# Performance work log

Hardware: AMD Instinct MI355X
Metric: run time of the kernel (lower is better)

The kernel has to match this reference:

```python
import jax, jax.numpy as jnp
import numpy as np

H = 16       # query heads
KV = 4       # key/value heads
HD = 256     # head dim
ROPE_THETA = 10000.0
EPS = 1e-6


def _rms_norm(x, w):
    # Gemma RMSNorm over last dim: x / rms * (1 + w), computed in fp32
    xf = x.astype(jnp.float32)
    var = jnp.mean(xf * xf, axis=-1, keepdims=True)
    out = xf * jax.lax.rsqrt(var + EPS) * (1.0 + w.astype(jnp.float32))
    return out.astype(x.dtype)


def _rope_cos_sin(position_ids):
    # cos/sin tables of shape [S, HD]
    inv_freq = 1.0 / (ROPE_THETA ** (jnp.arange(0, HD, 2, dtype=jnp.float32) / HD))
    ang = position_ids.astype(jnp.float32)[:, None] * inv_freq[None, :]  # [S, HD/2]
    emb = jnp.concatenate([ang, ang], axis=-1)                           # [S, HD]
    return jnp.cos(emb), jnp.sin(emb)


def _rotate_half(x):
    x1, x2 = jnp.split(x, 2, axis=-1)
    return jnp.concatenate([-x2, x1], axis=-1)


def _apply_rope(x, cos, sin):
    # x: [B, h, S, HD]; cos/sin: [S, HD] -> broadcast over batch and heads
    c = cos[None, None, :, :]
    s = sin[None, None, :, :]
    return (x * c + _rotate_half(x) * s).astype(x.dtype)


def setup_inputs() -> dict:
    key = jax.random.key(0)
    ks = jax.random.split(key, 8)
    B, S, D = 2, 2048, 2048
    inp = {
        "hidden_states": jax.random.normal(ks[0], (B, S, D), jnp.float32),
        "Wq": jax.random.normal(ks[1], (D, H * HD), jnp.float32) * 0.02,
        "Wk": jax.random.normal(ks[2], (D, KV * HD), jnp.float32) * 0.02,
        "Wv": jax.random.normal(ks[3], (D, KV * HD), jnp.float32) * 0.02,
        "Wo": jax.random.normal(ks[4], (H * HD, D), jnp.float32) * 0.02,
        "q_norm_w": jnp.zeros((HD,), jnp.float32),
        "k_norm_w": jnp.zeros((HD,), jnp.float32),
        "position_ids": jnp.arange(S, dtype=jnp.int32),
    }
    return inp


def reference(hidden_states, Wq, Wk, Wv, Wo, q_norm_w, k_norm_w, position_ids):
    B, S, D = hidden_states.shape
    scale = HD ** -0.5

    # projections -> [B, h, S, HD]
    q = jnp.einsum("bsd,de->bse", hidden_states, Wq).reshape(B, S, H, HD).transpose(0, 2, 1, 3)
    k = jnp.einsum("bsd,de->bse", hidden_states, Wk).reshape(B, S, KV, HD).transpose(0, 2, 1, 3)
    v = jnp.einsum("bsd,de->bse", hidden_states, Wv).reshape(B, S, KV, HD).transpose(0, 2, 1, 3)

    # Gemma per-head RMSNorm on q/k
    q = _rms_norm(q, q_norm_w)
    k = _rms_norm(k, k_norm_w)

    # RoPE
    cos, sin = _rope_cos_sin(position_ids)
    q = _apply_rope(q, cos, sin)
    k = _apply_rope(k, cos, sin)

    # GQA: repeat kv heads to match query heads
    rep = H // KV
    k = jnp.repeat(k, rep, axis=1)  # [B, H, S, HD]
    v = jnp.repeat(v, rep, axis=1)

    # SDPA with causal mask, softmax in fp32
    scores = jnp.einsum("bhqd,bhkd->bhqk", q, k) * scale
    causal = jnp.tril(jnp.ones((S, S), dtype=bool))
    scores = jnp.where(causal[None, None, :, :], scores, jnp.finfo(jnp.float32).min)
    probs = jax.nn.softmax(scores.astype(jnp.float32), axis=-1).astype(q.dtype)
    attn = jnp.einsum("bhqk,bhkd->bhqd", probs, v)  # [B, H, S, HD]

    attn = attn.transpose(0, 2, 1, 3).reshape(B, S, H * HD)
    return jnp.einsum("bse,ed->bsd", attn, Wo)
```

## Files before the change

kernel.cpp:

```cpp
#include <hip/hip_runtime.h>

typedef unsigned short ushort_t;
typedef __bf16 bf16_t;
typedef bf16_t bf16x8 __attribute__((ext_vector_type(8)));
typedef float floatx4 __attribute__((ext_vector_type(4)));
typedef ushort_t ushort4v __attribute__((ext_vector_type(4)));
typedef ushort_t ushort8v __attribute__((ext_vector_type(8)));

static constexpr int B = 2, S = 2048, D = 2048;
static constexpr int H = 16, KVH = 4, HD = 256;

#define DEVFN static __device__ __forceinline__

DEVFN ushort_t f2b(float f) {
  union { float f; unsigned u; } x; x.f = f;
  unsigned r = x.u + 0x7fffu + ((x.u >> 16) & 1u);
  return (ushort_t)(r >> 16);
}
DEVFN float b2f(ushort_t h) {
  union { unsigned u; float f; } x; x.u = ((unsigned)h) << 16;
  return x.f;
}
DEVFN void gll16(const void* g, void* l) {
  __builtin_amdgcn_global_load_lds(
      (const __attribute__((address_space(1))) void*)g,
      (__attribute__((address_space(3))) void*)l, 16, 0, 0);
}

DEVFN void bar() {
  asm volatile("" ::: "memory");
  __builtin_amdgcn_s_barrier();
  asm volatile("" ::: "memory");
}
template <int N>
DEVFN void waitvm() { asm volatile("s_waitcnt vmcnt(%0)" ::"n"(N) : "memory"); }

DEVFN ushort4v norm_rope_row(ushort4v raw, const float* __restrict__ w,
                             const float* __restrict__ tab, int s, float scale, int lane) {
  float v[4];
  float ss = 0.f;
#pragma unroll
  for (int i = 0; i < 4; i++) { v[i] = b2f(raw[i]); ss += v[i] * v[i]; }
#pragma unroll
  for (int m = 1; m < 64; m <<= 1) ss += __shfl_xor(ss, m, 64);
  const float inv = rsqrtf(ss * (1.0f / HD) + 1e-6f);
  float4 wv = *(const float4*)(w + lane * 4);
  float y[4];
  y[0] = v[0] * inv * (1.0f + wv.x);
  y[1] = v[1] * inv * (1.0f + wv.y);
  y[2] = v[2] * inv * (1.0f + wv.z);
  y[3] = v[3] * inv * (1.0f + wv.w);
  float py[4];
#pragma unroll
  for (int i = 0; i < 4; i++) py[i] = __shfl_xor(y[i], 32, 64);
  const bool lo = (lane < 32);
  ushort4v ov;
#pragma unroll
  for (int i = 0; i < 4; i++) {
    int dd = (lane * 4 + i) & 127;
    float2 cs = *(const float2*)(tab + ((size_t)s * 128 + dd) * 2);
    float rot = lo ? -py[i] : py[i];
    ov[i] = f2b((y[i] * cs.x + rot * cs.y) * scale);
  }
  return ov;
}

__global__ void k_cvt_bf16(const float* __restrict__ in, ushort_t* __restrict__ out, int n) {
  int i = (blockIdx.x * 256 + threadIdx.x) * 4;
  if (i >= n) return;
  float4 v = *(const float4*)(in + i);
  ushort4v o;
  o[0] = f2b(v.x); o[1] = f2b(v.y); o[2] = f2b(v.z); o[3] = f2b(v.w);
  *(ushort4v*)(out + i) = o;
}

__global__ void k_transpose_cvt(const float* __restrict__ in, ushort_t* __restrict__ out,
                                int R, int C) {
  __shared__ float tile[64][65];
  const int cb = blockIdx.x * 64, rb = blockIdx.y * 64;
  const int t = threadIdx.x;
  const int l16 = t & 15, g16 = t >> 4;
#pragma unroll
  for (int p = 0; p < 4; p++) {
    const int r = p * 16 + g16;
    float4 v = *(const float4*)(in + (size_t)(rb + r) * C + cb + l16 * 4);
    tile[r][l16 * 4 + 0] = v.x;
    tile[r][l16 * 4 + 1] = v.y;
    tile[r][l16 * 4 + 2] = v.z;
    tile[r][l16 * 4 + 3] = v.w;
  }
  __syncthreads();
#pragma unroll
  for (int p = 0; p < 4; p++) {
    const int c = p * 16 + g16;
    ushort4v o4;
#pragma unroll
    for (int i = 0; i < 4; i++) o4[i] = f2b(tile[l16 * 4 + i][c]);
    *(ushort4v*)(out + (size_t)(cb + c) * R + rb + l16 * 4) = o4;
  }
}

__global__ void k_rope_table(const int* __restrict__ pos_ids, float* __restrict__ tab) {
  int idx = blockIdx.x * 256 + threadIdx.x;
  int s = idx >> 7, dd = idx & 127;
  float ang = (float)pos_ids[s] * exp2f((float)dd * (-13.287712379549449f / 128.0f));
  tab[idx * 2] = cosf(ang);
  tab[idx * 2 + 1] = sinf(ang);
}

DEVFN void stage_tile(const ushort_t* __restrict__ A, const ushort_t* __restrict__ Bt,
                      ushort_t* smb, size_t arow0, size_t brow0, int K, int kt) {
  const int t = threadIdx.x;
  const int rq = t >> 2;
  const int cq = (t & 3) * 8;
#pragma unroll
  for (int i = 0; i < 2; i++) {
    const int cs = cq ^ ((rq & 8) << 1);
    gll16(A + (arow0 + rq) * (size_t)K + kt + i * 32 + cs, smb + i * 4096 + t * 8);
  }
#pragma unroll
  for (int i = 0; i < 4; i++) {
    const int row = ((i & 1) << 7) | rq;
    const int cs = cq ^ ((row & 8) << 1);
    gll16(Bt + (brow0 + row) * (size_t)K + kt + (i >> 1) * 32 + cs,
          smb + 8192 + i * 4096 + t * 8);
  }
}

DEVFN bf16x8 ldsA(const ushort_t* buf, int row, int ks, int lq) {
  const int c = (lq * 8) ^ ((row & 8) << 1);
  return *(const bf16x8*)(buf + ks * 4096 + row * 32 + c);
}
DEVFN bf16x8 ldsB(const ushort_t* buf, int row, int ks, int lq) {
  const int c = (lq * 8) ^ ((row & 8) << 1);
  return *(const bf16x8*)(buf + 8192 + ks * 8192 + row * 32 + c);
}

template <int MODE>
__global__ __launch_bounds__(512, 2)
void k_gemm256(const ushort_t* __restrict__ A, const ushort_t* __restrict__ Bt,
               void* __restrict__ C0, void* __restrict__ C1, void* __restrict__ C2,
               int N, int K) {
  __shared__ ushort_t sm[49152];
  const int tid = threadIdx.x;
  const int lane = tid & 63, wave = tid >> 6;
  const int lr = lane & 15, lq = lane >> 4;
  const int wm = wave >> 2, wn = wave & 3;
  const size_t m0 = (size_t)blockIdx.x * 128;
  const size_t n0 = (size_t)blockIdx.y * 256;

  floatx4 acc[4][4];
#pragma unroll
  for (int i = 0; i < 4; i++)
#pragma unroll
    for (int j = 0; j < 4; j++) acc[i][j] = {0.f, 0.f, 0.f, 0.f};

  const int NT = K >> 6;
  stage_tile(A, Bt, sm, m0, n0, K, 0);
  stage_tile(A, Bt, sm + 24576, m0, n0, K, 64);

  for (int t = 0; t < NT; ++t) {
    ushort_t* bA = sm + (t & 1) * 24576;
    if (t < NT - 1) waitvm<6>(); else waitvm<0>();
    bar();

    bf16x8 a[2][4], bfr[2][4];
#pragma unroll
    for (int ks = 0; ks < 2; ks++) {
#pragma unroll
      for (int m = 0; m < 4; m++) a[ks][m] = ldsA(bA, wm * 64 + m * 16 + lr, ks, lq);
#pragma unroll
      for (int n = 0; n < 4; n++) bfr[ks][n] = ldsB(bA, wn * 64 + n * 16 + lr, ks, lq);
    }
    __builtin_amdgcn_s_setprio(1);
#pragma unroll
    for (int m = 0; m < 4; m++)
#pragma unroll
      for (int n = 0; n < 4; n++)
        acc[m][n] = __builtin_amdgcn_mfma_f32_16x16x32_bf16(a[0][m], bfr[0][n], acc[m][n], 0, 0, 0);
    __builtin_amdgcn_s_setprio(0);
    asm volatile("s_waitcnt lgkmcnt(0)" ::: "memory");
    __builtin_amdgcn_sched_barrier(0);
    bar();
    if (t + 2 < NT) stage_tile(A, Bt, bA, m0, n0, K, (t + 2) * 64);
    __builtin_amdgcn_sched_barrier(0);
    __builtin_amdgcn_s_setprio(1);
#pragma unroll
    for (int m = 0; m < 4; m++)
#pragma unroll
      for (int n = 0; n < 4; n++)
        acc[m][n] = __builtin_amdgcn_mfma_f32_16x16x32_bf16(a[1][m], bfr[1][n], acc[m][n], 0, 0, 0);
    __builtin_amdgcn_s_setprio(0);
  }

  const int colb = (int)n0;
#pragma unroll
  for (int mg = 0; mg < 4; mg++)
#pragma unroll
    for (int ng = 0; ng < 4; ng++) {
      const size_t row0 = m0 + wm * 64 + mg * 16 + lq * 4;
      const int col = colb + wn * 64 + ng * 16 + lr;
      if (MODE == 1) {
#pragma unroll
        for (int r = 0; r < 4; r++)
          ((float*)C0)[(row0 + r) * N + col] = acc[mg][ng][r];
      } else {
        if (colb < 4096) {
#pragma unroll
          for (int r = 0; r < 4; r++)
            ((ushort_t*)C0)[(row0 + r) * 4096 + col] = f2b(acc[mg][ng][r]);
        } else if (colb < 5120) {
#pragma unroll
          for (int r = 0; r < 4; r++)
            ((ushort_t*)C1)[(row0 + r) * 1024 + (col - 4096)] = f2b(acc[mg][ng][r]);
        } else {
          const int ch = col - 5120;
          const int kvh = ch >> 8, chh = ch & 255, f = chh >> 4, lrv = chh & 15;
          const size_t bb = row0 >> 11;
          const int s0 = (int)(row0 & 2047);
          const int tile = s0 >> 6, kh = (s0 >> 5) & 1, lqv = (s0 >> 3) & 3, j0 = s0 & 7;
          ushort4v pk;
#pragma unroll
          for (int r = 0; r < 4; r++) pk[r] = f2b(acc[mg][ng][r]);
          *(ushort4v*)&((ushort_t*)C2)[((bb * KVH + kvh) * (S / 64) + tile) * 16384 +
                                       (size_t)(f * 2 + kh) * 512 +
                                       (size_t)(lqv * 16 + lrv) * 8 + j0] = pk;
        }
      }
    }
}

__global__ void k_norm_rope_k(const ushort_t* __restrict__ Kb, ushort_t* __restrict__ Kf,
                              const float* __restrict__ w, const float* __restrict__ tab) {
  __shared__ ushort_t t[64 * 264];
  const int lane = threadIdx.x & 63, wave = threadIdx.x >> 6;
  const int tile = blockIdx.x, kvh = blockIdx.y, b = blockIdx.z;
#pragma unroll
  for (int rr = 0; rr < 16; rr++) {
    const int row = wave * 16 + rr;
    const int s = tile * 64 + row;
    const ushort_t* p = Kb + ((size_t)(b * S + s) * KVH + kvh) * HD + lane * 4;
    ushort4v raw = *(const ushort4v*)p;
    *(ushort4v*)&t[row * 264 + lane * 4] = norm_rope_row(raw, w, tab, s, 1.0f, lane);
  }
  __syncthreads();
  ushort_t* dst = Kf + ((size_t)(b * KVH + kvh) * (S / 64) + tile) * 16384;
  const int lr = lane & 15, lq = lane >> 4;
#pragma unroll
  for (int q = 0; q < 8; q++) {
    const int c = wave * 8 + q;
    const int nt = c >> 3, ks = c & 7;
    ushort8v v = *(const ushort8v*)&t[(nt * 16 + lr) * 264 + ks * 32 + lq * 8];
    *(ushort8v*)&dst[(size_t)c * 512 + lane * 8] = v;
  }
}

__global__ __launch_bounds__(256, 2)
void k_attn(const ushort_t* __restrict__ Q, const ushort_t* __restrict__ Kf,
            const ushort_t* __restrict__ Vf, ushort_t* __restrict__ O,
            const float* __restrict__ qw, const float* __restrict__ tab) {
  __shared__ ushort_t Ks[32 * 512];
  __shared__ ushort_t Vs[32 * 512];
  __shared__ ushort_t Ps[4][16 * 72];
  const int lane = threadIdx.x & 63, wave = threadIdx.x >> 6;
  const int lr = lane & 15, lq = lane >> 4;
  const int lin = blockIdx.x;
  const int g = lin & 7, j = lin >> 3;
  const int b = g >> 2, kvh = g & 3;
  const int h = kvh * 4 + (j >> 4);
  const int xq = j & 15;
  const size_t kvb = (size_t)(b * KVH + kvh) * (S / 64);

#pragma unroll 1
  for (int half = 0; half < 2; half++) {
    const int qt = half ? xq : (S / 64 - 1 - xq);
    const int q0 = qt * 64 + wave * 16;
    const int sq = q0 + lr;

    bf16x8 qf[8];
    {
      const ushort_t* qp = Q + ((size_t)(b * S + sq) * H + h) * HD + lq * 8;
      ushort8v qr[8];
#pragma unroll
      for (int ks = 0; ks < 8; ks++) qr[ks] = *(const ushort8v*)(qp + ks * 32);
      float ss = 0.f;
#pragma unroll
      for (int ks = 0; ks < 8; ks++)
#pragma unroll
        for (int jj = 0; jj < 8; jj++) { float v = b2f(qr[ks][jj]); ss += v * v; }
      ss += __shfl_xor(ss, 16, 64);
      ss += __shfl_xor(ss, 32, 64);
      const float inv = rsqrtf(ss * (1.0f / HD) + 1e-6f);
      const float sc = 0.0625f * 1.4426950408889634f;
#pragma unroll
      for (int c = 0; c < 4; c++) {
        const int d0 = c * 32 + lq * 8;
        float wl[8], wh[8];
        {
          float4 a0 = *(const float4*)(qw + d0);
          float4 a1 = *(const float4*)(qw + d0 + 4);
          float4 a2 = *(const float4*)(qw + d0 + 128);
          float4 a3 = *(const float4*)(qw + d0 + 132);
          wl[0]=a0.x; wl[1]=a0.y; wl[2]=a0.z; wl[3]=a0.w;
          wl[4]=a1.x; wl[5]=a1.y; wl[6]=a1.z; wl[7]=a1.w;
          wh[0]=a2.x; wh[1]=a2.y; wh[2]=a2.z; wh[3]=a2.w;
          wh[4]=a3.x; wh[5]=a3.y; wh[6]=a3.z; wh[7]=a3.w;
        }
        const float* tp = tab + ((size_t)sq * 128 + d0) * 2;
        ushort8v olo, ohi;
#pragma unroll
        for (int jj = 0; jj < 8; jj++) {
          float ylo = b2f(qr[c][jj]) * inv * (1.0f + wl[jj]);
          float yhi = b2f(qr[c + 4][jj]) * inv * (1.0f + wh[jj]);
          float2 cs = *(const float2*)(tp + jj * 2);
          olo[jj] = f2b((ylo * cs.x - yhi * cs.y) * sc);
          ohi[jj] = f2b((yhi * cs.x + ylo * cs.y) * sc);
        }
        qf[c] = *reinterpret_cast<bf16x8*>(&olo);
        qf[c + 4] = *reinterpret_cast<bf16x8*>(&ohi);
      }
    }

    floatx4 o[16];
#pragma unroll
    for (int f = 0; f < 16; f++) o[f] = {0.f, 0.f, 0.f, 0.f};
    float m_i[4] = {-1e30f, -1e30f, -1e30f, -1e30f};
    float l_i[4] = {0.f, 0.f, 0.f, 0.f};

    const int ntiles = qt + 1;
    for (int kt = 0; kt < ntiles; kt++) {
      const int kbase = kt * 64;
      __syncthreads();
      const ushort_t* tb = Kf + (kvb + kt) * 16384;
      const ushort_t* vb = Vf + (kvb + kt) * 16384;
#pragma unroll
      for (int i = 0; i < 16; i++) {
        const int c = wave * 16 + i;
        if (c < 32) gll16(tb + (size_t)c * 512 + lane * 8, &Ks[c * 512 + lane * 8]);
        else        gll16(vb + (size_t)(c - 32) * 512 + lane * 8, &Vs[(c - 32) * 512 + lane * 8]);
      }
      __syncthreads();

      const int ntmax = min(4, ((q0 + 15 - kbase) >> 4) + 1);
      floatx4 sacc[4];
#pragma unroll
      for (int nt = 0; nt < 4; nt++) {
        if (nt < ntmax) {
          sacc[nt] = {0.f, 0.f, 0.f, 0.f};
#pragma unroll
          for (int ks = 0; ks < 8; ks++) {
            bf16x8 kf = *(const bf16x8*)&Ks[(nt * 8 + ks) * 512 + lane * 8];
            sacc[nt] = __builtin_amdgcn_mfma_f32_16x16x32_bf16(qf[ks], kf, sacc[nt], 0, 0, 0);
          }
        } else {
          sacc[nt] = {-1e30f, -1e30f, -1e30f, -1e30f};
        }
      }
      if (kbase + 63 > q0) {
#pragma unroll
        for (int nt = 0; nt < 4; nt++)
          if (nt < ntmax)
#pragma unroll
            for (int r = 0; r < 4; r++)
              if (kbase + nt * 16 + lr > q0 + lq * 4 + r) sacc[nt][r] = -1e30f;
      }
      float mt[4], alpha[4], rs[4];
#pragma unroll
      for (int r = 0; r < 4; r++)
        mt[r] = fmaxf(fmaxf(sacc[0][r], sacc[1][r]), fmaxf(sacc[2][r], sacc[3][r]));
#pragma unroll
      for (int m = 1; m < 16; m <<= 1)
#pragma unroll
        for (int r = 0; r < 4; r++) mt[r] = fmaxf(mt[r], __shfl_xor(mt[r], m, 64));
#pragma unroll
      for (int r = 0; r < 4; r++) {
        float mn = fmaxf(m_i[r], mt[r]);
        alpha[r] = exp2f(m_i[r] - mn);
        m_i[r] = mn;
      }
#pragma unroll
      for (int nt = 0; nt < 4; nt++)
#pragma unroll
        for (int r = 0; r < 4; r++) sacc[nt][r] = exp2f(sacc[nt][r] - m_i[r]);
#pragma unroll
      for (int r = 0; r < 4; r++)
        rs[r] = (sacc[0][r] + sacc[1][r]) + (sacc[2][r] + sacc[3][r]);
#pragma unroll
      for (int m = 1; m < 16; m <<= 1)
#pragma unroll
        for (int r = 0; r < 4; r++) rs[r] += __shfl_xor(rs[r], m, 64);
#pragma unroll
      for (int r = 0; r < 4; r++) l_i[r] = l_i[r] * alpha[r] + rs[r];
      if (__any((alpha[0] < 1.f) | (alpha[1] < 1.f) | (alpha[2] < 1.f) | (alpha[3] < 1.f))) {
#pragma unroll
        for (int f = 0; f < 16; f++) {
          o[f][0] *= alpha[0]; o[f][1] *= alpha[1];
          o[f][2] *= alpha[2]; o[f][3] *= alpha[3];
        }
      }
      ushort_t* psw = Ps[wave];
#pragma unroll
      for (int nt = 0; nt < 4; nt++)
#pragma unroll
        for (int r = 0; r < 4; r++)
          psw[(lq * 4 + r) * 72 + nt * 16 + lr] = f2b(sacc[nt][r]);
      bf16x8 pf0 = *(const bf16x8*)&psw[lr * 72 + lq * 8];
      bf16x8 pf1 = *(const bf16x8*)&psw[lr * 72 + 32 + lq * 8];
#pragma unroll
      for (int f = 0; f < 16; f++) {
        bf16x8 vf0 = *(const bf16x8*)&Vs[(f * 2 + 0) * 512 + lane * 8];
        o[f] = __builtin_amdgcn_mfma_f32_16x16x32_bf16(pf0, vf0, o[f], 0, 0, 0);
        bf16x8 vf1 = *(const bf16x8*)&Vs[(f * 2 + 1) * 512 + lane * 8];
        o[f] = __builtin_amdgcn_mfma_f32_16x16x32_bf16(pf1, vf1, o[f], 0, 0, 0);
      }
    }
    float invl[4];
#pragma unroll
    for (int r = 0; r < 4; r++) invl[r] = 1.0f / l_i[r];
#pragma unroll
    for (int f = 0; f < 16; f++)
#pragma unroll
      for (int r = 0; r < 4; r++)
        O[((size_t)(b * S + q0 + lq * 4 + r) * H + h) * HD + f * 16 + lr] =
            f2b(o[f][r] * invl[r]);
  }
}

extern "C" void kernel_launch(void* const* d_in, const int* in_sizes, int n_in,
                              void* d_out, int out_size, void* d_ws, size_t ws_size,
                              hipStream_t stream) {
  const float* hs = (const float*)d_in[0];
  const float* Wq = (const float*)d_in[1];
  const float* Wk = (const float*)d_in[2];
  const float* Wv = (const float*)d_in[3];
  const float* Wo = (const float*)d_in[4];
  const float* qw = (const float*)d_in[5];
  const float* kw = (const float*)d_in[6];
  const int* pos = (const int*)d_in[7];
  float* out = (float*)d_out;

  char* ws = (char*)d_ws;
  size_t off = 0;
  auto alloc = [&](size_t bytes) {
    void* p = ws + off;
    off += (bytes + 255) & ~(size_t)255;
    return p;
  };
  ushort_t* Xb   = (ushort_t*)alloc((size_t)B * S * D * 2);
  ushort_t* Wqt  = (ushort_t*)alloc((size_t)(H * HD) * D * 2);
  ushort_t* Wkvt = (ushort_t*)alloc((size_t)(2 * KVH * HD) * D * 2);
  ushort_t* Wot  = (ushort_t*)alloc((size_t)D * (H * HD) * 2);
  ushort_t* Qb   = (ushort_t*)alloc((size_t)B * S * H * HD * 2);
  ushort_t* Kf   = (ushort_t*)alloc((size_t)B * S * KVH * HD * 2);
  ushort_t* Vf   = (ushort_t*)alloc((size_t)B * S * KVH * HD * 2);
  ushort_t* Ab   = (ushort_t*)alloc((size_t)B * S * H * HD * 2);
  float*    tab  = (float*)alloc((size_t)S * 128 * 2 * sizeof(float));
  ushort_t* Kb = Ab;

  k_cvt_bf16<<<(B * S * D / 4 + 255) / 256, 256, 0, stream>>>(hs, Xb, B * S * D);
  k_transpose_cvt<<<dim3((H * HD) / 64, D / 64), 256, 0, stream>>>(Wq, Wqt, D, H * HD);
  k_transpose_cvt<<<dim3((KVH * HD) / 64, D / 64), 256, 0, stream>>>(Wk, Wkvt, D, KVH * HD);
  k_transpose_cvt<<<dim3((KVH * HD) / 64, D / 64), 256, 0, stream>>>(
      Wv, Wkvt + (size_t)(KVH * HD) * D, D, KVH * HD);
  k_transpose_cvt<<<dim3(D / 64, (H * HD) / 64), 256, 0, stream>>>(Wo, Wot, H * HD, D);
  k_rope_table<<<S * 128 / 256, 256, 0, stream>>>(pos, tab);

  k_gemm256<0><<<dim3((B * S) / 128, 6144 / 256), 512, 0, stream>>>(
      Xb, Wqt, Qb, Kb, Vf, 6144, D);

  k_norm_rope_k<<<dim3(S / 64, KVH, B), 256, 0, stream>>>(Kb, Kf, kw, tab);

  k_attn<<<512, 256, 0, stream>>>(Qb, Kf, Vf, Ab, qw, tab);

  k_gemm256<1><<<dim3((B * S) / 128, D / 256), 512, 0, stream>>>(
      Ab, Wot, out, nullptr, nullptr, D, H * HD);
}
```

Before: 505.1 us.

## Process two 16-row query fragments per wave to reuse each K/V tile

The attention kernel now gives each block a 128-row query tile, with each wave holding two 16-row Q fragments. Every K/V tile staged in LDS therefore feeds twice as many MFMAs, which halves K/V global-to-LDS traffic and barrier rounds per query row. The old loop that paired a long and a short causal tile inside one block is gone; each block now handles one tile chosen from a mirrored index. The cost is doubled accumulator and Q-fragment registers, which risks spills or lower occupancy, and less even per-block work under the causal mask.

```diff
diff --git a/kernel.cpp b/kernel.cpp
--- a/kernel.cpp
+++ b/kernel.cpp
@@ -265,164 +265,196 @@
   const int lane = threadIdx.x & 63, wave = threadIdx.x >> 6;
   const int lr = lane & 15, lq = lane >> 4;
   const int lin = blockIdx.x;
-  const int g = lin & 7, j = lin >> 3;
+  const int half_sel = lin >> 8;
+  const int r9 = lin & 255;
+  const int g = r9 & 7;
   const int b = g >> 2, kvh = g & 3;
-  const int h = kvh * 4 + (j >> 4);
-  const int xq = j & 15;
+  const int j = r9 >> 3;
+  const int h = kvh * 4 + (j >> 3);
+  const int p = j & 7;
+  const int qt = half_sel ? p : (15 - p);
   const size_t kvb = (size_t)(b * KVH + kvh) * (S / 64);
 
-#pragma unroll 1
-  for (int half = 0; half < 2; half++) {
-    const int qt = half ? xq : (S / 64 - 1 - xq);
-    const int q0 = qt * 64 + wave * 16;
-    const int sq = q0 + lr;
-
-    bf16x8 qf[8];
-    {
-      const ushort_t* qp = Q + ((size_t)(b * S + sq) * H + h) * HD + lq * 8;
-      ushort8v qr[8];
-#pragma unroll
-      for (int ks = 0; ks < 8; ks++) qr[ks] = *(const ushort8v*)(qp + ks * 32);
-      float ss = 0.f;
-#pragma unroll
-      for (int ks = 0; ks < 8; ks++)
-#pragma unroll
-        for (int jj = 0; jj < 8; jj++) { float v = b2f(qr[ks][jj]); ss += v * v; }
-      ss += __shfl_xor(ss, 16, 64);
-      ss += __shfl_xor(ss, 32, 64);
-      const float inv = rsqrtf(ss * (1.0f / HD) + 1e-6f);
-      const float sc = 0.0625f * 1.4426950408889634f;
-#pragma unroll
-      for (int c = 0; c < 4; c++) {
-        const int d0 = c * 32 + lq * 8;
-        float wl[8], wh[8];
-        {
-          float4 a0 = *(const float4*)(qw + d0);
-          float4 a1 = *(const float4*)(qw + d0 + 4);
-          float4 a2 = *(const float4*)(qw + d0 + 128);
-          float4 a3 = *(const float4*)(qw + d0 + 132);
-          wl[0]=a0.x; wl[1]=a0.y; wl[2]=a0.z; wl[3]=a0.w;
-          wl[4]=a1.x; wl[5]=a1.y; wl[6]=a1.z; wl[7]=a1.w;
-          wh[0]=a2.x; wh[1]=a2.y; wh[2]=a2.z; wh[3]=a2.w;
-          wh[4]=a3.x; wh[5]=a3.y; wh[6]=a3.z; wh[7]=a3.w;
+  const int q0 = qt * 128 + wave * 32;
+  const int ntiles = 2 * qt + 2;
+
+  bf16x8 qf[2][8];
+#pragma unroll
+  for (int rf = 0; rf < 2; rf++) {
+    const int sq = q0 + rf * 16 + lr;
+    const ushort_t* qp = Q + ((size_t)(b * S + sq) * H + h) * HD + lq * 8;
+    ushort8v qr[8];
+#pragma unroll
+    for (int ks = 0; ks < 8; ks++) qr[ks] = *(const ushort8v*)(qp + ks * 32);
+    float ss = 0.f;
+#pragma unroll
+    for (int ks = 0; ks < 8; ks++)
+#pragma unroll
+      for (int jj = 0; jj < 8; jj++) { float v = b2f(qr[ks][jj]); ss += v * v; }
+    ss += __shfl_xor(ss, 16, 64);
+    ss += __shfl_xor(ss, 32, 64);
+    const float inv = rsqrtf(ss * (1.0f / HD) + 1e-6f);
+    const float sc = 0.0625f * 1.4426950408889634f;
+#pragma unroll
+    for (int c = 0; c < 4; c++) {
+      const int d0 = c * 32 + lq * 8;
+      float wl[8], wh[8];
+      {
+        float4 a0 = *(const float4*)(qw + d0);
+        float4 a1 = *(const float4*)(qw + d0 + 4);
+        float4 a2 = *(const float4*)(qw + d0 + 128);
+        float4 a3 = *(const float4*)(qw + d0 + 132);
+        wl[0]=a0.x; wl[1]=a0.y; wl[2]=a0.z; wl[3]=a0.w;
+        wl[4]=a1.x; wl[5]=a1.y; wl[6]=a1.z; wl[7]=a1.w;
+        wh[0]=a2.x; wh[1]=a2.y; wh[2]=a2.z; wh[3]=a2.w;
+        wh[4]=a3.x; wh[5]=a3.y; wh[6]=a3.z; wh[7]=a3.w;
+      }
+      const float* tp = tab + ((size_t)sq * 128 + d0) * 2;
+      ushort8v olo, ohi;
+#pragma unroll
+      for (int jj = 0; jj < 8; jj++) {
+        float ylo = b2f(qr[c][jj]) * inv * (1.0f + wl[jj]);
+        float yhi = b2f(qr[c + 4][jj]) * inv * (1.0f + wh[jj]);
+        float2 cs = *(const float2*)(tp + jj * 2);
+        olo[jj] = f2b((ylo * cs.x - yhi * cs.y) * sc);
+        ohi[jj] = f2b((yhi * cs.x + ylo * cs.y) * sc);
+      }
+      qf[rf][c] = *reinterpret_cast<bf16x8*>(&olo);
+      qf[rf][c + 4] = *reinterpret_cast<bf16x8*>(&ohi);
+    }
+  }
+
+  floatx4 o[2][16];
+#pragma unroll
+  for (int rf = 0; rf < 2; rf++)
+#pragma unroll
+    for (int f = 0; f < 16; f++) o[rf][f] = {0.f, 0.f, 0.f, 0.f};
+  float m_i[2][4], l_i[2][4];
+#pragma unroll
+  for (int rf = 0; rf < 2; rf++)
+#pragma unroll
+    for (int r = 0; r < 4; r++) { m_i[rf][r] = -1e30f; l_i[rf][r] = 0.f; }
+
+  for (int kt = 0; kt < ntiles; kt++) {
+    const int kbase = kt * 64;
+    __syncthreads();
+    const ushort_t* tb = Kf + (kvb + kt) * 16384;
+    const ushort_t* vb = Vf + (kvb + kt) * 16384;
+#pragma unroll
+    for (int i = 0; i < 16; i++) {
+      const int c = wave * 16 + i;
+      if (c < 32) gll16(tb + (size_t)c * 512 + lane * 8, &Ks[c * 512 + lane * 8]);
+      else        gll16(vb + (size_t)(c - 32) * 512 + lane * 8, &Vs[(c - 32) * 512 + lane * 8]);
+    }
+    __syncthreads();
+
+    const int ntmax0 = min(4, ((q0 + 15 - kbase) >> 4) + 1);
+    const int ntmax1 = min(4, ((q0 + 31 - kbase) >> 4) + 1);
+    if (ntmax1 > 0) {
+      floatx4 sacc[2][4];
+#pragma unroll
+      for (int nt = 0; nt < 4; nt++) {
+        const bool a0 = nt < ntmax0, a1 = nt < ntmax1;
+        sacc[0][nt] = a0 ? floatx4{0.f, 0.f, 0.f, 0.f}
+                         : floatx4{-1e30f, -1e30f, -1e30f, -1e30f};
+        sacc[1][nt] = a1 ? floatx4{0.f, 0.f, 0.f, 0.f}
+                         : floatx4{-1e30f, -1e30f, -1e30f, -1e30f};
+        if (a1) {
+#pragma unroll
+          for (int ks = 0; ks < 8; ks++) {
+            bf16x8 kf = *(const bf16x8*)&Ks[(nt * 8 + ks) * 512 + lane * 8];
+            if (a0)
+              sacc[0][nt] = __builtin_amdgcn_mfma_f32_16x16x32_bf16(qf[0][ks], kf, sacc[0][nt], 0, 0, 0);
+            sacc[1][nt] = __builtin_amdgcn_mfma_f32_16x16x32_bf16(qf[1][ks], kf, sacc[1][nt], 0, 0, 0);
+          }
         }
-        const float* tp = tab + ((size_t)sq * 128 + d0) * 2;
-        ushort8v olo, ohi;
-#pragma unroll
-        for (int jj = 0; jj < 8; jj++) {
-          float ylo = b2f(qr[c][jj]) * inv * (1.0f + wl[jj]);
-          float yhi = b2f(qr[c + 4][jj]) * inv * (1.0f + wh[jj]);
-          float2 cs = *(const float2*)(tp + jj * 2);
-          olo[jj] = f2b((ylo * cs.x - yhi * cs.y) * sc);
-          ohi[jj] = f2b((yhi * cs.x + ylo * cs.y) * sc);
+      }
+      bf16x8 pf[2][2];
+      ushort_t* psw = Ps[wave];
+#pragma unroll
+      for (int rf = 0; rf < 2; rf++) {
+        const bool act = (rf == 0) ? (ntmax0 > 0) : true;
+        if (act) {
+          const int qb = q0 + rf * 16;
+          const int ntm = rf ? ntmax1 : ntmax0;
+          if (kbase + 63 > qb) {
+#pragma unroll
+            for (int nt = 0; nt < 4; nt++)
+              if (nt < ntm)
+#pragma unroll
+                for (int r = 0; r < 4; r++)
+                  if (kbase + nt * 16 + lr > qb + lq * 4 + r) sacc[rf][nt][r] = -1e30f;
+          }
+          float mt[4], alpha[4], rs[4];
+#pragma unroll
+          for (int r = 0; r < 4; r++)
+            mt[r] = fmaxf(fmaxf(sacc[rf][0][r], sacc[rf][1][r]),
+                          fmaxf(sacc[rf][2][r], sacc[rf][3][r]));
+#pragma unroll
+          for (int m = 1; m < 16; m <<= 1)
+#pragma unroll
+            for (int r = 0; r < 4; r++) mt[r] = fmaxf(mt[r], __shfl_xor(mt[r], m, 64));
+#pragma unroll
+          for (int r = 0; r < 4; r++) {
+            float mn = fmaxf(m_i[rf][r], mt[r]);
+            alpha[r] = exp2f(m_i[rf][r] - mn);
+            m_i[rf][r] = mn;
+          }
+#pragma unroll
+          for (int nt = 0; nt < 4; nt++)
+#pragma unroll
+            for (int r = 0; r < 4; r++) sacc[rf][nt][r] = exp2f(sacc[rf][nt][r] - m_i[rf][r]);
+#pragma unroll
+          for (int r = 0; r < 4; r++)
+            rs[r] = (sacc[rf][0][r] + sacc[rf][1][r]) + (sacc[rf][2][r] + sacc[rf][3][r]);
+#pragma unroll
+          for (int m = 1; m < 16; m <<= 1)
+#pragma unroll
+            for (int r = 0; r < 4; r++) rs[r] += __shfl_xor(rs[r], m, 64);
+#pragma unroll
+          for (int r = 0; r < 4; r++) l_i[rf][r] = l_i[rf][r] * alpha[r] + rs[r];
+          if (__any((alpha[0] < 1.f) | (alpha[1] < 1.f) | (alpha[2] < 1.f) | (alpha[3] < 1.f))) {
+#pragma unroll
+            for (int f = 0; f < 16; f++) {
+              o[rf][f][0] *= alpha[0]; o[rf][f][1] *= alpha[1];
+              o[rf][f][2] *= alpha[2]; o[rf][f][3] *= alpha[3];
+            }
+          }
+#pragma unroll
+          for (int nt = 0; nt < 4; nt++)
+#pragma unroll
+            for (int r = 0; r < 4; r++)
+              psw[(lq * 4 + r) * 72 + nt * 16 + lr] = f2b(sacc[rf][nt][r]);
+          pf[rf][0] = *(const bf16x8*)&psw[lr * 72 + lq * 8];
+          pf[rf][1] = *(const bf16x8*)&psw[lr * 72 + 32 + lq * 8];
         }
-        qf[c] = *reinterpret_cast<bf16x8*>(&olo);
-        qf[c + 4] = *reinterpret_cast<bf16x8*>(&ohi);
+      }
+      const bool act0 = (ntmax0 > 0);
+#pragma unroll
+      for (int f = 0; f < 16; f++) {
+        bf16x8 vf0 = *(const bf16x8*)&Vs[(f * 2 + 0) * 512 + lane * 8];
+        bf16x8 vf1 = *(const bf16x8*)&Vs[(f * 2 + 1) * 512 + lane * 8];
+        if (act0) {
+          o[0][f] = __builtin_amdgcn_mfma_f32_16x16x32_bf16(pf[0][0], vf0, o[0][f], 0, 0, 0);
+          o[0][f] = __builtin_amdgcn_mfma_f32_16x16x32_bf16(pf[0][1], vf1, o[0][f], 0, 0, 0);
+        }
+        o[1][f] = __builtin_amdgcn_mfma_f32_16x16x32_bf16(pf[1][0], vf0, o[1][f], 0, 0, 0);
+        o[1][f] = __builtin_amdgcn_mfma_f32_16x16x32_bf16(pf[1][1], vf1, o[1][f], 0, 0, 0);
       }
     }
-
-    floatx4 o[16];
-#pragma unroll
-    for (int f = 0; f < 16; f++) o[f] = {0.f, 0.f, 0.f, 0.f};
-    float m_i[4] = {-1e30f, -1e30f, -1e30f, -1e30f};
-    float l_i[4] = {0.f, 0.f, 0.f, 0.f};
-
-    const int ntiles = qt + 1;
-    for (int kt = 0; kt < ntiles; kt++) {
-      const int kbase = kt * 64;
-      __syncthreads();
-      const ushort_t* tb = Kf + (kvb + kt) * 16384;
-      const ushort_t* vb = Vf + (kvb + kt) * 16384;
-#pragma unroll
-      for (int i = 0; i < 16; i++) {
-        const int c = wave * 16 + i;
-        if (c < 32) gll16(tb + (size_t)c * 512 + lane * 8, &Ks[c * 512 + lane * 8]);
-        else        gll16(vb + (size_t)(c - 32) * 512 + lane * 8, &Vs[(c - 32) * 512 + lane * 8]);
-      }
-      __syncthreads();
-
-      const int ntmax = min(4, ((q0 + 15 - kbase) >> 4) + 1);
-      floatx4 sacc[4];
-#pragma unroll
-      for (int nt = 0; nt < 4; nt++) {
-        if (nt < ntmax) {
-          sacc[nt] = {0.f, 0.f, 0.f, 0.f};
-#pragma unroll
-          for (int ks = 0; ks < 8; ks++) {
-            bf16x8 kf = *(const bf16x8*)&Ks[(nt * 8 + ks) * 512 + lane * 8];
-            sacc[nt] = __builtin_amdgcn_mfma_f32_16x16x32_bf16(qf[ks], kf, sacc[nt], 0, 0, 0);
-          }
-        } else {
-          sacc[nt] = {-1e30f, -1e30f, -1e30f, -1e30f};
-        }
-      }
-      if (kbase + 63 > q0) {
-#pragma unroll
-        for (int nt = 0; nt < 4; nt++)
-          if (nt < ntmax)
-#pragma unroll
-            for (int r = 0; r < 4; r++)
-              if (kbase + nt * 16 + lr > q0 + lq * 4 + r) sacc[nt][r] = -1e30f;
-      }
-      float mt[4], alpha[4], rs[4];
+  }
+
+#pragma unroll
+  for (int rf = 0; rf < 2; rf++) {
+    float invl[4];
+#pragma unroll
+    for (int r = 0; r < 4; r++) invl[r] = 1.0f / l_i[rf][r];
+#pragma unroll
+    for (int f = 0; f < 16; f++)
 #pragma unroll
       for (int r = 0; r < 4; r++)
-        mt[r] = fmaxf(fmaxf(sacc[0][r], sacc[1][r]), fmaxf(sacc[2][r], sacc[3][r]));
-#pragma unroll
-      for (int m = 1; m < 16; m <<= 1)
-#pragma unroll
-        for (int r = 0; r < 4; r++) mt[r] = fmaxf(mt[r], __shfl_xor(mt[r], m, 64));
-#pragma unroll
-      for (int r = 0; r < 4; r++) {
-        float mn = fmaxf(m_i[r], mt[r]);
-        alpha[r] = exp2f(m_i[r] - mn);
-        m_i[r] = mn;
-      }
-#pragma unroll
-      for (int nt = 0; nt < 4; nt++)
-#pragma unroll
-        for (int r = 0; r < 4; r++) sacc[nt][r] = exp2f(sacc[nt][r] - m_i[r]);
-#pragma unroll
-      for (int r = 0; r < 4; r++)
-        rs[r] = (sacc[0][r] + sacc[1][r]) + (sacc[2][r] + sacc[3][r]);
-#pragma unroll
-      for (int m = 1; m < 16; m <<= 1)
-#pragma unroll
-        for (int r = 0; r < 4; r++) rs[r] += __shfl_xor(rs[r], m, 64);
-#pragma unroll
-      for (int r = 0; r < 4; r++) l_i[r] = l_i[r] * alpha[r] + rs[r];
-      if (__any((alpha[0] < 1.f) | (alpha[1] < 1.f) | (alpha[2] < 1.f) | (alpha[3] < 1.f))) {
-#pragma unroll
-        for (int f = 0; f < 16; f++) {
-          o[f][0] *= alpha[0]; o[f][1] *= alpha[1];
-          o[f][2] *= alpha[2]; o[f][3] *= alpha[3];
-        }
-      }
-      ushort_t* psw = Ps[wave];
-#pragma unroll
-      for (int nt = 0; nt < 4; nt++)
-#pragma unroll
-        for (int r = 0; r < 4; r++)
-          psw[(lq * 4 + r) * 72 + nt * 16 + lr] = f2b(sacc[nt][r]);
-      bf16x8 pf0 = *(const bf16x8*)&psw[lr * 72 + lq * 8];
-      bf16x8 pf1 = *(const bf16x8*)&psw[lr * 72 + 32 + lq * 8];
-#pragma unroll
-      for (int f = 0; f < 16; f++) {
-        bf16x8 vf0 = *(const bf16x8*)&Vs[(f * 2 + 0) * 512 + lane * 8];
-        o[f] = __builtin_amdgcn_mfma_f32_16x16x32_bf16(pf0, vf0, o[f], 0, 0, 0);
-        bf16x8 vf1 = *(const bf16x8*)&Vs[(f * 2 + 1) * 512 + lane * 8];
-        o[f] = __builtin_amdgcn_mfma_f32_16x16x32_bf16(pf1, vf1, o[f], 0, 0, 0);
-      }
-    }
-    float invl[4];
-#pragma unroll
-    for (int r = 0; r < 4; r++) invl[r] = 1.0f / l_i[r];
-#pragma unroll
-    for (int f = 0; f < 16; f++)
-#pragma unroll
-      for (int r = 0; r < 4; r++)
-        O[((size_t)(b * S + q0 + lq * 4 + r) * H + h) * HD + f * 16 + lr] =
-            f2b(o[f][r] * invl[r]);
+        O[((size_t)(b * S + q0 + rf * 16 + lq * 4 + r) * H + h) * HD + f * 16 + lr] =
+            f2b(o[rf][f][r] * invl[r]);
   }
 }
 
```

Measured after the change: 747.7 us. 1.48x slower.
